# Performance work log

Hardware: AMD Instinct MI355X
Metric: run time of the kernel (lower is better)

## Reference

```python
import jax, jax.numpy as jnp
import numpy as np

HEAD = 8

def setup_inputs() -> dict:
    key = jax.random.key(0)
    k1, k2 = jax.random.split(key)
    B, S, D = 4, 2048, 512
    x = jax.random.normal(k1, (B, S, D), dtype=jnp.float32)
    Wq = jax.random.normal(k2, (D, D), dtype=jnp.float32) * (1.0 / np.sqrt(D))
    return {"x": x, "Wq": Wq}


def reference(x, Wq):
    # Faithful to source: Q, K, V all use linear_q (bug preserved).
    B, S, D = x.shape
    hd = D // HEAD
    q = jnp.einsum('bsd,de->bse', x, Wq)
    # Q = K = V = q
    qh = q.reshape(B, S, HEAD, hd).transpose(0, 2, 1, 3)  # [B,H,S,hd]
    # scale by sqrt(head_dim): inputs.shape[-1] inside ScaleDotAttentionLayer
    scores = jnp.einsum('bhqd,bhkd->bhqk', qh, qh) / jnp.sqrt(jnp.float32(hd))
    weights = jax.nn.softmax(scores, axis=-1)
    ctx = jnp.einsum('bhqk,bhkd->bhqd', weights, qh)
    out = ctx.transpose(0, 2, 1, 3).reshape(B, S, D)
    return out
```

## Files before the change

### kernel.cpp

```cpp
#include <hip/hip_runtime.h>
#include <hip/hip_fp16.h>
#include <math.h>

#define SS 2048
#define DD 512
#define NH 8
#define HD 64

typedef __attribute__((ext_vector_type(8))) short frag_ab;
typedef __attribute__((ext_vector_type(4))) float frag_cd;
typedef __attribute__((ext_vector_type(4))) _Float16 frag_b4;

static __device__ inline unsigned int pack_h2(float x, float y) {
    __half2 t = __floats2half2_rn(x, y);
    return *(unsigned int*)&t;
}

__global__ __launch_bounds__(512, 4) void gemm_kernel(const float* __restrict__ x,
                                                      const float* __restrict__ w,
                                                      unsigned short* __restrict__ q) {
    __shared__ __align__(16) unsigned short Ah[2][128 * 72];
    __shared__ __align__(16) unsigned short Bt[2][64 * 72];
    const int tid = threadIdx.x;
    const int lane = tid & 63, wv = tid >> 6;
    const int a = lane & 15, g = lane >> 4;
    const int bm = blockIdx.x, bn = blockIdx.y;
    const int wr = wv >> 1, wc = wv & 1;

    frag_cd acc[2][2] = {};
    const int ar = tid >> 4;
    const int ac = (tid & 15) * 4;
    const int bnw = tid & 63;
    const int bc  = tid >> 6;
    const int bp  = (bc + 2 * (bnw & 7)) & 7;

    float4 av[4];
    float  bw[8];

    auto load_tiles = [&](int k0) {
        #pragma unroll
        for (int i = 0; i < 4; ++i)
            av[i] = *(const float4*)(x + (size_t)(bm * 128 + ar + 32 * i) * 512 + k0 + ac);
        #pragma unroll
        for (int j = 0; j < 8; ++j)
            bw[j] = w[(size_t)(k0 + bc * 8 + j) * 512 + bn * 64 + bnw];
    };
    auto stage_tiles = [&](int buf) {
        #pragma unroll
        for (int i = 0; i < 4; ++i) {
            uint2 hh = { pack_h2(av[i].x, av[i].y), pack_h2(av[i].z, av[i].w) };
            *(uint2*)&Ah[buf][(ar + 32 * i) * 72 + ac] = hh;
        }
        unsigned int tb[4];
        #pragma unroll
        for (int j = 0; j < 4; ++j)
            tb[j] = pack_h2(bw[2 * j], bw[2 * j + 1]);
        *(uint4*)&Bt[buf][bnw * 72 + bp * 8] = *(uint4*)tb;
    };

    load_tiles(0);
    stage_tiles(0);
    load_tiles(64);
    __syncthreads();

    for (int it = 0; it < 8; ++it) {
        const int cur = it & 1;
        if (it < 7) stage_tiles(cur ^ 1);
        if (it < 6) load_tiles((it + 2) * 64);
        #pragma unroll
        for (int kh = 0; kh < 2; ++kh) {
            frag_ab bf[2], af[2];
            #pragma unroll
            for (int nt = 0; nt < 2; ++nt) {
                const int nr = wc * 32 + nt * 16 + a;
                const int pr = ((kh * 4 + g) + 2 * (nr & 7)) & 7;
                bf[nt] = *(const frag_ab*)&Bt[cur][nr * 72 + pr * 8];
            }
            #pragma unroll
            for (int mt = 0; mt < 2; ++mt)
                af[mt] = *(const frag_ab*)&Ah[cur][(wr * 32 + mt * 16 + a) * 72 + kh * 32 + g * 8];
            #pragma unroll
            for (int mt = 0; mt < 2; ++mt)
                #pragma unroll
                for (int nt = 0; nt < 2; ++nt)
                    acc[mt][nt] = __builtin_amdgcn_mfma_f32_16x16x32_f16(af[mt], bf[nt], acc[mt][nt], 0, 0, 0);
        }
        __syncthreads();
    }
    #pragma unroll
    for (int mt = 0; mt < 2; ++mt)
        #pragma unroll
        for (int nt = 0; nt < 2; ++nt)
            #pragma unroll
            for (int r = 0; r < 4; ++r) {
                const int m = bm * 128 + wr * 32 + mt * 16 + g * 4 + r;
                const int n = bn * 64 + wc * 32 + nt * 16 + a;
                __half hv = __float2half_rn(acc[mt][nt][r]);
                q[(size_t)m * 512 + n] = *(unsigned short*)&hv;
            }
}

__global__ __launch_bounds__(512, 4) void attn_kernel(const __half* __restrict__ qg,
                                                      float* __restrict__ out) {
    __shared__ __align__(16) unsigned char LDSB[69632];
    unsigned short* KtB = (unsigned short*)LDSB;
    unsigned short* VtB = (unsigned short*)(LDSB + 36864);

    const int tid = threadIdx.x;
    const int lane = tid & 63, wv = tid >> 6;
    const int a = lane & 15, g = lane >> 4;
    const int qq = wv & 3;
    const int kv = wv >> 2;
    const int bid = blockIdx.x;
    const int slab = bid & 31;
    const int qt = bid >> 5;
    const int h  = slab & 7;
    const int b  = slab >> 3;

    const unsigned short* qbh = (const unsigned short*)qg + (size_t)b * SS * DD + h * HD;
    const int qrow0 = qt * 128 + qq * 32;

    frag_ab qf[2][2];
    const __half2 qsc = __float2half2_rn(0.18033688011112042f);
    #pragma unroll
    for (int nt = 0; nt < 2; ++nt)
        #pragma unroll
        for (int kh = 0; kh < 2; ++kh) {
            frag_ab t = *(const frag_ab*)(qbh + (size_t)(qrow0 + nt * 16 + a) * DD + kh * 32 + g * 8);
            __half2* phh = (__half2*)&t;
            #pragma unroll
            for (int i = 0; i < 4; ++i) phh[i] = __hmul2(phh[i], qsc);
            qf[nt][kh] = t;
        }

    frag_cd oacc[4][2] = {};
    float lsum[2] = {0.f, 0.f};

    const int t8 = tid & 255;
    const int f0 = (t8 & 31) * 2;
    const int u8 = t8 >> 5;
    const int r0 = u8 * 8;
    const int keybase = (tid >> 8) * 1024;
    unsigned short* KsBase = KtB + (tid >> 8) * 4608;
    unsigned short* VsBase = VtB + (tid >> 8) * 4096;
    const int vsw = (u8 ^ (t8 & 7)) << 3;

    unsigned int d[8];
    #pragma unroll
    for (int k = 0; k < 8; ++k)
        d[k] = *(const unsigned int*)(qbh + (size_t)(keybase + r0 + k) * DD + f0);

    const unsigned short* KcBase = KtB + kv * 4608;
    const unsigned short* VcBase = VtB + kv * 4096;
    const float coff = -11.541560327111707f;
    const int sv = (a >> 1) & 7;

    auto stage_write = [&](int buf) {
        unsigned short* Ksb = KsBase + buf * 9216;
        unsigned short* Vsb = VsBase + buf * 8192;
        #pragma unroll
        for (int k = 0; k < 8; ++k)
            *(unsigned int*)&Ksb[(r0 + k) * 72 + f0] = d[k];
        unsigned int vlo[4], vhi[4];
        #pragma unroll
        for (int j = 0; j < 4; ++j) {
            vlo[j] = (d[2 * j] & 0xFFFFu) | (d[2 * j + 1] << 16);
            vhi[j] = (d[2 * j] >> 16)     | (d[2 * j + 1] & 0xFFFF0000u);
        }
        *(uint4*)&Vsb[f0 * 64 + vsw]       = *(uint4*)vlo;
        *(uint4*)&Vsb[(f0 + 1) * 64 + vsw] = *(uint4*)vhi;
    };

    stage_write(0);
    #pragma unroll
    for (int k = 0; k < 8; ++k)
        d[k] = *(const unsigned int*)(qbh + (size_t)(keybase + 64 + r0 + k) * DD + f0);
    __syncthreads();

    for (int it = 0; it < 16; ++it) {
        const int cur = it & 1;
        if (it < 15) stage_write(cur ^ 1);
        if (it < 14) {
            const int kb = keybase + (it + 2) * 64;
            #pragma unroll
            for (int k = 0; k < 8; ++k)
                d[k] = *(const unsigned int*)(qbh + (size_t)(kb + r0 + k) * DD + f0);
        }
        const unsigned short* Kc = KcBase + cur * 9216;
        const unsigned short* Vc = VcBase + cur * 8192;

        #pragma unroll
        for (int kt = 0; kt < 4; ++kt) {
            const frag_ab ka0 = *(const frag_ab*)&Kc[(kt * 16 + a) * 72 + g * 8];
            const frag_ab ka1 = *(const frag_ab*)&Kc[(kt * 16 + a) * 72 + 32 + g * 8];
            frag_b4 pbk[2];
            #pragma unroll
            for (int nt = 0; nt < 2; ++nt) {
                frag_cd c = {coff, coff, coff, coff};
                c = __builtin_amdgcn_mfma_f32_16x16x32_f16(ka0, qf[nt][0], c, 0, 0, 0);
                c = __builtin_amdgcn_mfma_f32_16x16x32_f16(ka1, qf[nt][1], c, 0, 0, 0);
                const float p0 = __builtin_amdgcn_exp2f(c[0]);
                const float p1 = __builtin_amdgcn_exp2f(c[1]);
                const float p2 = __builtin_amdgcn_exp2f(c[2]);
                const float p3 = __builtin_amdgcn_exp2f(c[3]);
                lsum[nt] += (p0 + p1) + (p2 + p3);
                union { unsigned int u[2]; frag_b4 hh; } pu;
                pu.u[0] = pack_h2(p0, p1);
                pu.u[1] = pack_h2(p2, p3);
                pbk[nt] = pu.hh;
            }
            const int vch = ((2 * kt + (g >> 1)) ^ sv) << 3;
            const int vof = (g & 1) << 2;
            #pragma unroll
            for (int ft = 0; ft < 4; ++ft) {
                const frag_b4 va = *(const frag_b4*)&Vc[(ft * 16 + a) * 64 + vch + vof];
                oacc[ft][0] = __builtin_amdgcn_mfma_f32_16x16x16f16(va, pbk[0], oacc[ft][0], 0, 0, 0);
                oacc[ft][1] = __builtin_amdgcn_mfma_f32_16x16x16f16(va, pbk[1], oacc[ft][1], 0, 0, 0);
            }
        }
        __syncthreads();
    }

    #pragma unroll
    for (int nt = 0; nt < 2; ++nt) {
        lsum[nt] += __shfl_xor(lsum[nt], 16, 64);
        lsum[nt] += __shfl_xor(lsum[nt], 32, 64);
    }
    float* Obuf = (float*)LDSB;
    float* Lbuf = (float*)(LDSB + 33792);
    if (kv == 1) {
        #pragma unroll
        for (int ft = 0; ft < 4; ++ft)
            #pragma unroll
            for (int nt = 0; nt < 2; ++nt)
                #pragma unroll
                for (int r = 0; r < 4; ++r)
                    Obuf[qq * 2112 + (ft * 16 + g * 4 + r) * 33 + nt * 16 + a] = oacc[ft][nt][r];
        if (g == 0)
            #pragma unroll
            for (int nt = 0; nt < 2; ++nt)
                Lbuf[qq * 32 + nt * 16 + a] = lsum[nt];
    }
    __syncthreads();
    if (kv == 0) {
        #pragma unroll
        for (int nt = 0; nt < 2; ++nt) {
            const float inv = 1.f / (lsum[nt] + Lbuf[qq * 32 + nt * 16 + a]);
            float* op = out + ((size_t)b * SS + qrow0 + nt * 16 + a) * DD + h * HD;
            #pragma unroll
            for (int ft = 0; ft < 4; ++ft) {
                const int fb = ft * 16 + g * 4;
                float4 vv = {
                    (oacc[ft][nt][0] + Obuf[qq * 2112 + (fb + 0) * 33 + nt * 16 + a]) * inv,
                    (oacc[ft][nt][1] + Obuf[qq * 2112 + (fb + 1) * 33 + nt * 16 + a]) * inv,
                    (oacc[ft][nt][2] + Obuf[qq * 2112 + (fb + 2) * 33 + nt * 16 + a]) * inv,
                    (oacc[ft][nt][3] + Obuf[qq * 2112 + (fb + 3) * 33 + nt * 16 + a]) * inv };
                *(float4*)(op + fb) = vv;
            }
        }
    }
}

extern "C" void kernel_launch(void* const* d_in, const int* in_sizes, int n_in,
                              void* d_out, int out_size, void* d_ws, size_t ws_size,
                              hipStream_t stream) {
    const float* x  = (const float*)d_in[0];
    const float* wq = (const float*)d_in[1];
    float* out = (float*)d_out;
    unsigned short* q_h = (unsigned short*)d_ws;

    dim3 ggrid(64, 8);
    gemm_kernel<<<ggrid, 512, 0, stream>>>(x, wq, q_h);
    attn_kernel<<<512, 512, 0, stream>>>((const __half*)q_h, out);
}
```

Measured before the change: 120.8 us.

## Load K fragments directly from global memory, single-buffer V in LDS

K tiles are no longer staged through LDS. Each wave loads its K MFMA fragments straight from global memory, one subtile ahead, and only V is written to LDS, now single-buffered. This cuts LDS footprint from about 68KB to about 34KB, which may allow more resident blocks, and removes the K LDS writes and reads. The cost is a second barrier per iteration, no overlap between the V staging writes and compute, and per-wave global K loads that rely on L2/L1 hits.

```diff
diff --git a/kernel.cpp b/kernel.cpp
--- a/kernel.cpp
+++ b/kernel.cpp
@@ -102,9 +102,8 @@
 
 __global__ __launch_bounds__(512, 4) void attn_kernel(const __half* __restrict__ qg,
                                                       float* __restrict__ out) {
-    __shared__ __align__(16) unsigned char LDSB[69632];
-    unsigned short* KtB = (unsigned short*)LDSB;
-    unsigned short* VtB = (unsigned short*)(LDSB + 36864);
+    __shared__ __align__(16) unsigned char LDSB[34304];
+    unsigned short* VtB = (unsigned short*)LDSB;
 
     const int tid = threadIdx.x;
     const int lane = tid & 63, wv = tid >> 6;
@@ -141,8 +140,7 @@
     const int u8 = t8 >> 5;
     const int r0 = u8 * 8;
     const int keybase = (tid >> 8) * 1024;
-    unsigned short* KsBase = KtB + (tid >> 8) * 4608;
-    unsigned short* VsBase = VtB + (tid >> 8) * 4096;
+    unsigned short* Vs = VtB + (tid >> 8) * 4096;
     const int vsw = (u8 ^ (t8 & 7)) << 3;
 
     unsigned int d[8];
@@ -150,55 +148,43 @@
     for (int k = 0; k < 8; ++k)
         d[k] = *(const unsigned int*)(qbh + (size_t)(keybase + r0 + k) * DD + f0);
 
-    const unsigned short* KcBase = KtB + kv * 4608;
-    const unsigned short* VcBase = VtB + kv * 4096;
+    const unsigned short* Vc = VtB + kv * 4096;
     const float coff = -11.541560327111707f;
     const int sv = (a >> 1) & 7;
 
-    auto stage_write = [&](int buf) {
-        unsigned short* Ksb = KsBase + buf * 9216;
-        unsigned short* Vsb = VsBase + buf * 8192;
-        #pragma unroll
-        for (int k = 0; k < 8; ++k)
-            *(unsigned int*)&Ksb[(r0 + k) * 72 + f0] = d[k];
-        unsigned int vlo[4], vhi[4];
-        #pragma unroll
-        for (int j = 0; j < 4; ++j) {
-            vlo[j] = (d[2 * j] & 0xFFFFu) | (d[2 * j + 1] << 16);
-            vhi[j] = (d[2 * j] >> 16)     | (d[2 * j + 1] & 0xFFFF0000u);
-        }
-        *(uint4*)&Vsb[f0 * 64 + vsw]       = *(uint4*)vlo;
-        *(uint4*)&Vsb[(f0 + 1) * 64 + vsw] = *(uint4*)vhi;
-    };
-
-    stage_write(0);
-    #pragma unroll
-    for (int k = 0; k < 8; ++k)
-        d[k] = *(const unsigned int*)(qbh + (size_t)(keybase + 64 + r0 + k) * DD + f0);
-    __syncthreads();
+    const unsigned short* kptr = qbh + (size_t)(kv * 1024 + a) * DD + g * 8;
+    frag_ab kc0 = *(const frag_ab*)(kptr);
+    frag_ab kc1 = *(const frag_ab*)(kptr + 32);
 
     for (int it = 0; it < 16; ++it) {
-        const int cur = it & 1;
-        if (it < 15) stage_write(cur ^ 1);
-        if (it < 14) {
-            const int kb = keybase + (it + 2) * 64;
+        __syncthreads();
+        {
+            unsigned int vlo[4], vhi[4];
+            #pragma unroll
+            for (int j = 0; j < 4; ++j) {
+                vlo[j] = (d[2 * j] & 0xFFFFu) | (d[2 * j + 1] << 16);
+                vhi[j] = (d[2 * j] >> 16)     | (d[2 * j + 1] & 0xFFFF0000u);
+            }
+            *(uint4*)&Vs[f0 * 64 + vsw]       = *(uint4*)vlo;
+            *(uint4*)&Vs[(f0 + 1) * 64 + vsw] = *(uint4*)vhi;
+        }
+        __syncthreads();
+
+        if (it + 1 < 16) {
+            const int kb = keybase + (it + 1) * 64;
             #pragma unroll
             for (int k = 0; k < 8; ++k)
                 d[k] = *(const unsigned int*)(qbh + (size_t)(kb + r0 + k) * DD + f0);
         }
-        const unsigned short* Kc = KcBase + cur * 9216;
-        const unsigned short* Vc = VcBase + cur * 8192;
 
         #pragma unroll
         for (int kt = 0; kt < 4; ++kt) {
-            const frag_ab ka0 = *(const frag_ab*)&Kc[(kt * 16 + a) * 72 + g * 8];
-            const frag_ab ka1 = *(const frag_ab*)&Kc[(kt * 16 + a) * 72 + 32 + g * 8];
             frag_b4 pbk[2];
             #pragma unroll
             for (int nt = 0; nt < 2; ++nt) {
                 frag_cd c = {coff, coff, coff, coff};
-                c = __builtin_amdgcn_mfma_f32_16x16x32_f16(ka0, qf[nt][0], c, 0, 0, 0);
-                c = __builtin_amdgcn_mfma_f32_16x16x32_f16(ka1, qf[nt][1], c, 0, 0, 0);
+                c = __builtin_amdgcn_mfma_f32_16x16x32_f16(kc0, qf[nt][0], c, 0, 0, 0);
+                c = __builtin_amdgcn_mfma_f32_16x16x32_f16(kc1, qf[nt][1], c, 0, 0, 0);
                 const float p0 = __builtin_amdgcn_exp2f(c[0]);
                 const float p1 = __builtin_amdgcn_exp2f(c[1]);
                 const float p2 = __builtin_amdgcn_exp2f(c[2]);
@@ -209,6 +195,11 @@
                 pu.u[1] = pack_h2(p2, p3);
                 pbk[nt] = pu.hh;
             }
+            if (!(it == 15 && kt == 3)) {
+                const int noff = (kt < 3) ? (it * 64 + (kt + 1) * 16) : ((it + 1) * 64);
+                kc0 = *(const frag_ab*)(kptr + (size_t)noff * DD);
+                kc1 = *(const frag_ab*)(kptr + (size_t)noff * DD + 32);
+            }
             const int vch = ((2 * kt + (g >> 1)) ^ sv) << 3;
             const int vof = (g & 1) << 2;
             #pragma unroll
@@ -218,7 +209,6 @@
                 oacc[ft][1] = __builtin_amdgcn_mfma_f32_16x16x16f16(va, pbk[1], oacc[ft][1], 0, 0, 0);
             }
         }
-        __syncthreads();
     }
 
     #pragma unroll
@@ -226,6 +216,7 @@
         lsum[nt] += __shfl_xor(lsum[nt], 16, 64);
         lsum[nt] += __shfl_xor(lsum[nt], 32, 64);
     }
+    __syncthreads();
     float* Obuf = (float*)LDSB;
     float* Lbuf = (float*)(LDSB + 33792);
     if (kv == 1) {
```

Measured after the change: 141.8 us. +17.4%, slower.
